# Optimization experiments

Hardware: AMD Instinct MI355X
Metric: run time of the kernel (lower is better)

The kernel has to match this reference:

```python
import jax, jax.numpy as jnp
import numpy as np

M_LOCAL = 100000
N_GLOBAL = 50000
C = 128
E = 1600000
EDGE_DIM = 16
BN_EPS = 1e-5


def setup_inputs() -> dict:
    key = jax.random.key(0)
    ks = jax.random.split(key, 12)
    s = 1.0 / np.sqrt(C)
    inp = {
        "h_local": jax.random.normal(ks[0], (M_LOCAL, C), jnp.float32),
        "h_global": jax.random.normal(ks[1], (N_GLOBAL, C), jnp.float32),
        "ea_flat": jax.random.normal(ks[2], (E, EDGE_DIM), jnp.float32),
        # GIN MLP: Linear(C,C) -> ReLU -> Linear(C,C)
        "W1": jax.random.normal(ks[3], (C, C), jnp.float32) * s,
        "b1": jnp.zeros((C,), jnp.float32),
        "W2": jax.random.normal(ks[4], (C, C), jnp.float32) * s,
        "b2": jnp.zeros((C,), jnp.float32),
        "eps": jnp.zeros((), jnp.float32),  # GIN train_eps, init 0
        "gamma_l": jnp.ones((C,), jnp.float32),
        "beta_l": jnp.zeros((C,), jnp.float32),
        "gamma_g": jnp.ones((C,), jnp.float32),
        "beta_g": jnp.zeros((C,), jnp.float32),
        "intra_ei": jax.random.randint(ks[5], (2, E), 0, M_LOCAL, jnp.int32),
        "node_ids": jax.random.randint(ks[6], (M_LOCAL,), 0, N_GLOBAL, jnp.int32),
        "valid": jnp.ones((M_LOCAL,), jnp.bool_),
        "N_total": N_GLOBAL,
    }
    return inp


def _batchnorm(x, gamma, beta):
    # training-mode BN: biased batch statistics over node dim
    mu = jnp.mean(x, axis=0)
    var = jnp.mean((x - mu) ** 2, axis=0)
    return (x - mu) * jax.lax.rsqrt(var + BN_EPS) * gamma + beta


def reference(h_local, h_global, ea_flat, W1, b1, W2, b2, eps,
              gamma_l, beta_l, gamma_g, beta_g,
              intra_ei, node_ids, valid, N_total):
    M = h_local.shape[0]
    valid_f = valid.astype(h_local.dtype)[:, None]
    clamped = jnp.maximum(node_ids, 0)

    # inject global context, zero padding
    h_in = (h_local + h_global[clamped]) * valid_f

    # GINConv: mlp((1+eps)*x + sum_{j->i} x_j)   (ea_flat unused for 'gin')
    src, dst = intra_ei[0], intra_ei[1]
    agg = jax.ops.segment_sum(h_in[src], dst, num_segments=M)
    pre = (1.0 + eps) * h_in + agg
    h_local_new = jnp.maximum(pre @ W1 + b1, 0.0) @ W2 + b2
    h_local_new = h_local_new * valid_f

    # cross-subgraph consensus: scatter mean into global nodes
    h_sum = jax.ops.segment_sum(h_local_new, clamped, num_segments=N_total)
    v_cnt = jax.ops.segment_sum(valid_f[:, 0], clamped, num_segments=N_total)
    h_global_new = h_sum / jnp.maximum(v_cnt, 1.0)[:, None]

    # local track: BN + residual (Identity since in==out) + mask (dropout p=0)
    h_local_new = _batchnorm(h_local_new, gamma_l, beta_l) + h_local
    h_local_new = h_local_new * valid_f

    # global track: BN + residual
    h_global_new = _batchnorm(h_global_new, gamma_g, beta_g) + h_global

    return (h_local_new, h_global_new)
```

## Files before the change

### kernel.cpp

```cpp
#include <hip/hip_runtime.h>

#define CDIM 128
#define NBE 3125
#define NBN 391
#define SMAXE 1024
#define SMAXN 512
#define CHUNK 16384
#define H1LD 136

typedef __bf16 bf16x8 __attribute__((ext_vector_type(8)));
typedef __bf16 bf16x4 __attribute__((ext_vector_type(4)));
typedef float f32x4 __attribute__((ext_vector_type(4)));

__global__ __launch_bounds__(256) void k_init(
    const float* __restrict__ hl, const float* __restrict__ hg,
    const int* __restrict__ nid, __bf16* __restrict__ h_in,
    const float* __restrict__ W1, const float* __restrict__ W2,
    __bf16* __restrict__ Wt1, __bf16* __restrict__ Wt2, int M, int gInit)
{
    int bid = blockIdx.x;
    if (bid >= gInit) {
        int idx = (bid - gInit) * 256 + threadIdx.x;
        int k = idx >> 7, n = idx & 127;
        Wt1[n * CDIM + k] = (__bf16)W1[k * CDIM + n];
        Wt2[n * CDIM + k] = (__bf16)W2[k * CDIM + n];
        return;
    }
    int idx = bid * 256 + threadIdx.x;
    if (idx >= M * 16) return;
    int i = idx >> 4, q8 = idx & 15;
    int g = max(nid[i], 0);
    const float4* hl4 = reinterpret_cast<const float4*>(hl);
    const float4* hg4 = reinterpret_cast<const float4*>(hg);
    float4 a0 = hl4[i * 32 + q8 * 2], a1 = hl4[i * 32 + q8 * 2 + 1];
    float4 b0 = hg4[g * 32 + q8 * 2], b1 = hg4[g * 32 + q8 * 2 + 1];
    bf16x8 o;
    o[0] = (__bf16)(a0.x + b0.x); o[1] = (__bf16)(a0.y + b0.y);
    o[2] = (__bf16)(a0.z + b0.z); o[3] = (__bf16)(a0.w + b0.w);
    o[4] = (__bf16)(a1.x + b1.x); o[5] = (__bf16)(a1.y + b1.y);
    o[6] = (__bf16)(a1.z + b1.z); o[7] = (__bf16)(a1.w + b1.w);
    *reinterpret_cast<bf16x8*>(&h_in[(size_t)i * CDIM + q8 * 8]) = o;
}

__global__ __launch_bounds__(256) void k_count(
    const int* __restrict__ ei, const int* __restrict__ nid,
    int* __restrict__ bcnt, int E, int M)
{
    __shared__ int lh[4608];
    int t = threadIdx.x;
    for (int i = t; i < 4608; i += 256) lh[i] = 0;
    __syncthreads();
    int stride = gridDim.x * 256;
    for (int e = blockIdx.x * 256 + t; e < E; e += stride)
        atomicAdd(&lh[ei[E + e] >> 5], 1);
    for (int i = blockIdx.x * 256 + t; i < M; i += stride)
        atomicAdd(&lh[4096 + (max(nid[i], 0) >> 7)], 1);
    __syncthreads();
    for (int i = t; i < 4608; i += 256)
        if (lh[i]) atomicAdd(&bcnt[i], lh[i]);
}

__global__ __launch_bounds__(1024) void k_scan(
    const int* __restrict__ bcnt, int* __restrict__ bboff_e,
    int* __restrict__ bboff_n, int* __restrict__ bcur)
{
    __shared__ int sh[1024];
    int t = threadIdx.x;
    int v0 = bcnt[4 * t], v1 = bcnt[4 * t + 1], v2 = bcnt[4 * t + 2], v3 = bcnt[4 * t + 3];
    int s = v0 + v1 + v2 + v3;
    sh[t] = s;
    __syncthreads();
    for (int st = 1; st < 1024; st <<= 1) {
        int a = (t >= st) ? sh[t - st] : 0;
        __syncthreads();
        sh[t] += a;
        __syncthreads();
    }
    int acc = sh[t] - s;
    bboff_e[4 * t] = acc; bcur[4 * t] = acc; acc += v0;
    bboff_e[4 * t + 1] = acc; bcur[4 * t + 1] = acc; acc += v1;
    bboff_e[4 * t + 2] = acc; bcur[4 * t + 2] = acc; acc += v2;
    bboff_e[4 * t + 3] = acc; bcur[4 * t + 3] = acc; acc += v3;
    if (t == 1023) bboff_e[4096] = acc;
    __syncthreads();
    int v = (t < 512) ? bcnt[4096 + t] : 0;
    sh[t] = v;
    __syncthreads();
    for (int st = 1; st < 1024; st <<= 1) {
        int a = (t >= st) ? sh[t - st] : 0;
        __syncthreads();
        sh[t] += a;
        __syncthreads();
    }
    int ex = sh[t] - v;
    if (t < 512) { bboff_n[t] = ex; bcur[4096 + t] = ex; }
    if (t == 511) bboff_n[512] = ex + v;
}

__global__ __launch_bounds__(256) void k_bscatter(
    const int* __restrict__ ei, const int* __restrict__ nid,
    int* __restrict__ bcur, int* __restrict__ packed_e,
    int* __restrict__ packed_n, int E, int M)
{
    __shared__ int lh[4608];
    int t = threadIdx.x;
    int e0 = blockIdx.x * CHUNK;
    int n = min(CHUNK, E - e0);
    for (int i = t; i < 4608; i += 256) lh[i] = 0;
    __syncthreads();
    for (int j = t; j < n; j += 256)
        atomicAdd(&lh[ei[E + e0 + j] >> 5], 1);
    for (int i = blockIdx.x * 256 + t; i < M; i += gridDim.x * 256)
        atomicAdd(&lh[4096 + (max(nid[i], 0) >> 7)], 1);
    __syncthreads();
    for (int i = t; i < 4608; i += 256) {
        int c = lh[i];
        if (c) lh[i] = atomicAdd(&bcur[i], c);
    }
    __syncthreads();
    for (int j = t; j < n; j += 256) {
        int s = ei[e0 + j], d = ei[E + e0 + j];
        int pos = atomicAdd(&lh[d >> 5], 1);
        packed_e[pos] = s | ((d & 31) << 17);
    }
    for (int i = blockIdx.x * 256 + t; i < M; i += gridDim.x * 256) {
        int g = max(nid[i], 0);
        int pos = atomicAdd(&lh[4096 + (g >> 7)], 1);
        packed_n[pos] = i | ((g & 127) << 17);
    }
}

__global__ __launch_bounds__(256) void k_agg_fused(
    const __bf16* __restrict__ h_in, const int* __restrict__ packed,
    const int* __restrict__ bboff, const float* __restrict__ epsp,
    __bf16* __restrict__ pre, int M)
{
    __shared__ int lsrc[SMAXE];
    __shared__ int lcnt[32], lbase[32], lpos[32];
    int t = threadIdx.x;
    int b = blockIdx.x;
    int base = bboff[b];
    int n = min(bboff[b + 1] - base, SMAXE);
    if (t < 32) lcnt[t] = 0;
    __syncthreads();
    for (int j = t; j < n; j += 256)
        atomicAdd(&lcnt[packed[base + j] >> 17], 1);
    __syncthreads();
    if (t == 0) {
        int acc = 0;
        for (int i = 0; i < 32; ++i) { int c = lcnt[i]; lbase[i] = acc; lpos[i] = acc; acc += c; }
    }
    __syncthreads();
    for (int j = t; j < n; j += 256) {
        int p = packed[base + j];
        int r = atomicAdd(&lpos[p >> 17], 1);
        lsrc[r] = p & 0x1FFFF;
    }
    __syncthreads();

    float es = 1.0f + epsp[0];
    int slot = t >> 4, q = t & 15;
    int r0 = b * 32;
#pragma unroll
    for (int rr0 = 0; rr0 < 2; ++rr0) {
        int rr = slot + rr0 * 16;
        int row = r0 + rr;
        if (row >= M) break;
        bf16x8 a = *reinterpret_cast<const bf16x8*>(&h_in[(size_t)row * CDIM + q * 8]);
        float f[8];
#pragma unroll
        for (int k2 = 0; k2 < 8; ++k2) f[k2] = es * (float)a[k2];
        int sb = lbase[rr], cnt = lcnt[rr];
        int j = 0;
        for (; j + 1 < cnt; j += 2) {
            int s0 = lsrc[sb + j], s1 = lsrc[sb + j + 1];
            bf16x8 u0 = *reinterpret_cast<const bf16x8*>(&h_in[(size_t)s0 * CDIM + q * 8]);
            bf16x8 u1 = *reinterpret_cast<const bf16x8*>(&h_in[(size_t)s1 * CDIM + q * 8]);
#pragma unroll
            for (int k2 = 0; k2 < 8; ++k2) f[k2] += (float)u0[k2] + (float)u1[k2];
        }
        if (j < cnt) {
            int s0 = lsrc[sb + j];
            bf16x8 u0 = *reinterpret_cast<const bf16x8*>(&h_in[(size_t)s0 * CDIM + q * 8]);
#pragma unroll
            for (int k2 = 0; k2 < 8; ++k2) f[k2] += (float)u0[k2];
        }
        bf16x8 o;
#pragma unroll
        for (int k2 = 0; k2 < 8; ++k2) o[k2] = (__bf16)f[k2];
        *reinterpret_cast<bf16x8*>(&pre[(size_t)row * CDIM + q * 8]) = o;
    }
}

__global__ __launch_bounds__(256) void k_mlp(
    const __bf16* __restrict__ pre, const __bf16* __restrict__ Wt1,
    const __bf16* __restrict__ Wt2, const float* __restrict__ b1,
    const float* __restrict__ b2, __bf16* __restrict__ y,
    float* __restrict__ part, int M)
{
    __shared__ bf16x8 w_lds4[2048];
    __shared__ __bf16 h1t[64 * H1LD];
    __shared__ float pst[256];
    int t = threadIdx.x;
#pragma unroll
    for (int j = 0; j < 8; ++j) {
        int c = t + j * 256;
        int n = c >> 4, cr = c & 15, kc = cr >> 2, g = cr & 3;
        w_lds4[((n >> 4) * 4 + kc) * 64 + g * 16 + (n & 15)] =
            reinterpret_cast<const bf16x8*>(Wt1)[c];
    }
    if (t < 256) pst[t] = 0.f;
    __syncthreads();

    int wave = t >> 6, lane = t & 63;
    int r0 = blockIdx.x * 64 + wave * 16;
    int srcrow = min(r0 + (lane & 15), M - 1);
    int krow = (lane >> 4) * 8;
    int col = lane & 15;

    bf16x8 a[4];
#pragma unroll
    for (int kc = 0; kc < 4; ++kc)
        a[kc] = *reinterpret_cast<const bf16x8*>(
            &pre[(size_t)srcrow * CDIM + kc * 32 + krow]);

    f32x4 acc1[8] = {};
#pragma unroll
    for (int kc = 0; kc < 4; ++kc)
#pragma unroll
        for (int nt = 0; nt < 8; ++nt)
            acc1[nt] = __builtin_amdgcn_mfma_f32_16x16x32_bf16(
                a[kc], w_lds4[(nt * 4 + kc) * 64 + lane], acc1[nt], 0, 0, 0);

    int lrowb = wave * 16 + (lane >> 4) * 4;
#pragma unroll
    for (int nt = 0; nt < 8; ++nt) {
        float bv = b1[nt * 16 + col];
#pragma unroll
        for (int reg = 0; reg < 4; ++reg) {
            float v = fmaxf(acc1[nt][reg] + bv, 0.f);
            h1t[(lrowb + reg) * H1LD + nt * 16 + col] = (__bf16)v;
        }
    }
    __syncthreads();

#pragma unroll
    for (int j = 0; j < 8; ++j) {
        int c = t + j * 256;
        int n = c >> 4, cr = c & 15, kc = cr >> 2, g = cr & 3;
        w_lds4[((n >> 4) * 4 + kc) * 64 + g * 16 + (n & 15)] =
            reinterpret_cast<const bf16x8*>(Wt2)[c];
    }
    __syncthreads();

    int lrow = wave * 16 + (lane & 15);
    bf16x8 a2[4];
#pragma unroll
    for (int kc = 0; kc < 4; ++kc)
        a2[kc] = *reinterpret_cast<const bf16x8*>(&h1t[lrow * H1LD + kc * 32 + krow]);

    f32x4 acc2[8] = {};
#pragma unroll
    for (int kc = 0; kc < 4; ++kc)
#pragma unroll
        for (int nt = 0; nt < 8; ++nt)
            acc2[nt] = __builtin_amdgcn_mfma_f32_16x16x32_bf16(
                a2[kc], w_lds4[(nt * 4 + kc) * 64 + lane], acc2[nt], 0, 0, 0);

    int rowbase = r0 + (lane >> 4) * 4;
#pragma unroll
    for (int nt = 0; nt < 8; ++nt) {
        float bv = b2[nt * 16 + col];
        float s = 0.f, s2 = 0.f;
#pragma unroll
        for (int reg = 0; reg < 4; ++reg) {
            int row = rowbase + reg;
            float v = acc2[nt][reg] + bv;
            if (row < M) {
                y[(size_t)row * CDIM + nt * 16 + col] = (__bf16)v;
                s += v;
                s2 = fmaf(v, v, s2);
            }
        }
        s += __shfl_xor(s, 16); s += __shfl_xor(s, 32);
        s2 += __shfl_xor(s2, 16); s2 += __shfl_xor(s2, 32);
        if ((lane >> 4) == 0) {
            atomicAdd(&pst[nt * 16 + col], s);
            atomicAdd(&pst[128 + nt * 16 + col], s2);
        }
    }
    __syncthreads();
    if (t < 256) part[(size_t)blockIdx.x * 256 + t] = pst[t];
}

__global__ __launch_bounds__(256) void k_gmean(
    const __bf16* __restrict__ y, const int* __restrict__ packed,
    const int* __restrict__ bboff, float* __restrict__ out_g,
    float* __restrict__ part, int N)
{
    __shared__ int lrows[SMAXN];
    __shared__ int lcnt[32], lbase[32], lpos[32];
    __shared__ float pst[256];
    int t = threadIdx.x;
    int b = blockIdx.x >> 2;
    int quarter = blockIdx.x & 3;
    int base = bboff[b];
    int n = min(bboff[b + 1] - base, SMAXN);
    if (t < 32) lcnt[t] = 0;
    if (t < 256) pst[t] = 0.f;
    __syncthreads();
    for (int j = t; j < n; j += 256) {
        int ld = packed[base + j] >> 17;
        if ((ld >> 5) == quarter) atomicAdd(&lcnt[ld & 31], 1);
    }
    __syncthreads();
    if (t == 0) {
        int acc = 0;
        for (int i = 0; i < 32; ++i) { int c = lcnt[i]; lbase[i] = acc; lpos[i] = acc; acc += c; }
    }
    __syncthreads();
    for (int j = t; j < n; j += 256) {
        int p = packed[base + j];
        int ld = p >> 17;
        if ((ld >> 5) == quarter) {
            int r = atomicAdd(&lpos[ld & 31], 1);
            lrows[r] = p & 0x1FFFF;
        }
    }
    __syncthreads();

    int slot = t >> 4, q = t & 15;
    int g0 = b * 128 + quarter * 32;
    float csum[8] = {}, csq[8] = {};
#pragma unroll
    for (int rr0 = 0; rr0 < 2; ++rr0) {
        int rr = slot + rr0 * 16;
        int g = g0 + rr;
        if (g >= N) break;
        float f[8] = {};
        int sb = lbase[rr], cnt = lcnt[rr];
        for (int j = 0; j < cnt; ++j) {
            int r = lrows[sb + j];
            bf16x8 v = *reinterpret_cast<const bf16x8*>(&y[(size_t)r * CDIM + q * 8]);
#pragma unroll
            for (int k2 = 0; k2 < 8; ++k2) f[k2] += (float)v[k2];
        }
        float inv = 1.0f / fmaxf((float)cnt, 1.0f);
        float4 o0, o1;
        o0.x = f[0] * inv; o0.y = f[1] * inv; o0.z = f[2] * inv; o0.w = f[3] * inv;
        o1.x = f[4] * inv; o1.y = f[5] * inv; o1.z = f[6] * inv; o1.w = f[7] * inv;
        float* dst = out_g + (size_t)g * CDIM + q * 8;
        *reinterpret_cast<float4*>(dst) = o0;
        *reinterpret_cast<float4*>(dst + 4) = o1;
        float m[8] = {o0.x, o0.y, o0.z, o0.w, o1.x, o1.y, o1.z, o1.w};
#pragma unroll
        for (int k2 = 0; k2 < 8; ++k2) {
            csum[k2] += m[k2];
            csq[k2] = fmaf(m[k2], m[k2], csq[k2]);
        }
    }
#pragma unroll
    for (int k2 = 0; k2 < 8; ++k2) {
        atomicAdd(&pst[q * 8 + k2], csum[k2]);
        atomicAdd(&pst[128 + q * 8 + k2], csq[k2]);
    }
    __syncthreads();
    if (t < 256) part[(size_t)blockIdx.x * 256 + t] = pst[t];
}

__global__ __launch_bounds__(256) void k_reduce_scale(
    const float* __restrict__ part_l, int nl,
    const float* __restrict__ part_g, int ng,
    const float* __restrict__ gl, const float* __restrict__ bl,
    const float* __restrict__ gg, const float* __restrict__ bg,
    float* __restrict__ sc, int M, int N)
{
    int c = blockIdx.x;
    bool isL = c < 128;
    const float* part = isL ? part_l : part_g;
    int n = isL ? nl : ng;
    int col = isL ? c : c - 128;
    int t = threadIdx.x;
    float s1 = 0.f, s2 = 0.f;
    for (int i = t; i < n; i += 256) {
        const float* row = part + (size_t)i * 256;
        s1 += row[col];
        s2 += row[128 + col];
    }
    __shared__ float sh1[256], sh2[256];
    sh1[t] = s1; sh2[t] = s2;
    __syncthreads();
    for (int w = 128; w > 0; w >>= 1) {
        if (t < w) { sh1[t] += sh1[t + w]; sh2[t] += sh2[t + w]; }
        __syncthreads();
    }
    if (t == 0) {
        float cnt = isL ? (float)M : (float)N;
        float mu = sh1[0] / cnt;
        float var = sh2[0] / cnt - mu * mu;
        float gamma = isL ? gl[col] : gg[col];
        float beta  = isL ? bl[col] : bg[col];
        float sca = gamma * rsqrtf(var + 1e-5f);
        int off = isL ? 0 : 256;
        sc[off + col] = sca;
        sc[off + 128 + col] = beta - mu * sca;
    }
}

__global__ __launch_bounds__(256) void k_fin(
    const __bf16* __restrict__ y, const float* __restrict__ hl,
    float* __restrict__ out_l, float* __restrict__ out_g,
    const float* __restrict__ hg, const float* __restrict__ sc,
    int M, int N, int gFinL)
{
    int bid = blockIdx.x;
    if (bid < gFinL) {
        int idx = bid * 256 + threadIdx.x;
        if (idx >= M * 32) return;
        int q = idx & 31;
        float4 s4 = reinterpret_cast<const float4*>(sc)[q];
        float4 h4 = reinterpret_cast<const float4*>(sc + 128)[q];
        bf16x4 v = *reinterpret_cast<const bf16x4*>(&y[(size_t)idx * 4]);
        float4 r = reinterpret_cast<const float4*>(hl)[idx];
        reinterpret_cast<float4*>(out_l)[idx] = make_float4(
            fmaf((float)v[0], s4.x, h4.x) + r.x, fmaf((float)v[1], s4.y, h4.y) + r.y,
            fmaf((float)v[2], s4.z, h4.z) + r.z, fmaf((float)v[3], s4.w, h4.w) + r.w);
    } else {
        int idx = (bid - gFinL) * 256 + threadIdx.x;
        if (idx >= N * 32) return;
        int q = idx & 31;
        float4 s4 = reinterpret_cast<const float4*>(sc + 256)[q];
        float4 h4 = reinterpret_cast<const float4*>(sc + 384)[q];
        float4 v = reinterpret_cast<float4*>(out_g)[idx];
        float4 r = reinterpret_cast<const float4*>(hg)[idx];
        reinterpret_cast<float4*>(out_g)[idx] = make_float4(
            fmaf(v.x, s4.x, h4.x) + r.x, fmaf(v.y, s4.y, h4.y) + r.y,
            fmaf(v.z, s4.z, h4.z) + r.z, fmaf(v.w, s4.w, h4.w) + r.w);
    }
}

extern "C" void kernel_launch(void* const* d_in, const int* in_sizes, int n_in,
                              void* d_out, int out_size, void* d_ws, size_t ws_size,
                              hipStream_t stream)
{
    const float* h_local  = (const float*)d_in[0];
    const float* h_global = (const float*)d_in[1];
    const float* W1   = (const float*)d_in[3];
    const float* b1   = (const float*)d_in[4];
    const float* W2   = (const float*)d_in[5];
    const float* b2   = (const float*)d_in[6];
    const float* eps  = (const float*)d_in[7];
    const float* gl   = (const float*)d_in[8];
    const float* bl   = (const float*)d_in[9];
    const float* gg   = (const float*)d_in[10];
    const float* bg   = (const float*)d_in[11];
    const int*   ei   = (const int*)d_in[12];
    const int*   nid  = (const int*)d_in[13];

    const int M = in_sizes[13];
    const int N = in_sizes[1] / CDIM;
    const int E = in_sizes[12] / 2;
    const int gGemm = (M + 63) / 64;
    const int nGm   = NBN * 4;

    float* out_l = (float*)d_out;
    float* out_g = out_l + (size_t)M * CDIM;

    __bf16* pre = (__bf16*)d_out;

    char* odf = (char*)d_out + 26000000;
    int* packed_n = (int*)odf;
    int* bcnt     = packed_n + M;
    int* bboff_e  = bcnt + 4608;
    int* bboff_n  = bboff_e + 4097;
    int* bcur     = bboff_n + 513;
    float* part_l = (float*)((char*)d_out + 28000000);
    float* part_g = part_l + (size_t)gGemm * 256;

    int* packed_e = (int*)out_g;

    __bf16* h_in = (__bf16*)d_ws;
    __bf16* y    = (__bf16*)((char*)d_ws + 25600000);
    char*  wst   = (char*)d_ws + 51200000;
    __bf16* Wt1  = (__bf16*)wst;
    __bf16* Wt2  = Wt1 + CDIM * CDIM;
    float* sc    = (float*)(Wt2 + CDIM * CDIM);

    hipMemsetAsync(bcnt, 0, 4608 * sizeof(int), stream);

    int gInit = (M * 16 + 255) / 256;
    k_init<<<gInit + 64, 256, 0, stream>>>(h_local, h_global, nid, h_in,
                                           W1, W2, Wt1, Wt2, M, gInit);

    k_count<<<256, 256, 0, stream>>>(ei, nid, bcnt, E, M);
    k_scan<<<1, 1024, 0, stream>>>(bcnt, bboff_e, bboff_n, bcur);

    int gBS = (E + CHUNK - 1) / CHUNK;
    k_bscatter<<<gBS, 256, 0, stream>>>(ei, nid, bcur, packed_e, packed_n, E, M);

    k_agg_fused<<<NBE, 256, 0, stream>>>(h_in, packed_e, bboff_e, eps, pre, M);

    k_mlp<<<gGemm, 256, 0, stream>>>(pre, Wt1, Wt2, b1, b2, y, part_l, M);

    k_gmean<<<nGm, 256, 0, stream>>>(y, packed_n, bboff_n, out_g, part_g, N);

    k_reduce_scale<<<256, 256, 0, stream>>>(part_l, gGemm, part_g, nGm,
                                            gl, bl, gg, bg, sc, M, N);

    int gFinL = (M * 32 + 255) / 256;
    int gFinG = (N * 32 + 255) / 256;
    k_fin<<<gFinL + gFinG, 256, 0, stream>>>(y, h_local, out_l, out_g,
                                             h_global, sc, M, N, gFinL);
}
```

Before: 279.0 us.

## Replace count-scan bucketing with fixed-capacity bucket slots in a single scatter pass

Removes the separate histogram-count and prefix-scan kernels. Edges and node ids are now scattered straight into fixed-capacity bucket slots (1024 per destination bucket, 512 per global-node bucket), and the atomic cursors double as bucket counts for the aggregation and mean kernels. The scatter kernel also moves to 1024-thread blocks with half-size chunks. This saves two launches and a full extra pass over the edge destination indices. The cost is a sparser layout, and any bucket that exceeds its capacity silently drops entries, which the earlier code also clamped.

```diff
diff --git a/kernel.cpp b/kernel.cpp
--- a/kernel.cpp
+++ b/kernel.cpp
@@ -3,9 +3,9 @@
 #define CDIM 128
 #define NBE 3125
 #define NBN 391
-#define SMAXE 1024
-#define SMAXN 512
-#define CHUNK 16384
+#define CAPE 1024
+#define CAPN 512
+#define CHUNK 8192
 #define H1LD 136
 
 typedef __bf16 bf16x8 __attribute__((ext_vector_type(8)));
@@ -42,62 +42,7 @@
     *reinterpret_cast<bf16x8*>(&h_in[(size_t)i * CDIM + q8 * 8]) = o;
 }
 
-__global__ __launch_bounds__(256) void k_count(
-    const int* __restrict__ ei, const int* __restrict__ nid,
-    int* __restrict__ bcnt, int E, int M)
-{
-    __shared__ int lh[4608];
-    int t = threadIdx.x;
-    for (int i = t; i < 4608; i += 256) lh[i] = 0;
-    __syncthreads();
-    int stride = gridDim.x * 256;
-    for (int e = blockIdx.x * 256 + t; e < E; e += stride)
-        atomicAdd(&lh[ei[E + e] >> 5], 1);
-    for (int i = blockIdx.x * 256 + t; i < M; i += stride)
-        atomicAdd(&lh[4096 + (max(nid[i], 0) >> 7)], 1);
-    __syncthreads();
-    for (int i = t; i < 4608; i += 256)
-        if (lh[i]) atomicAdd(&bcnt[i], lh[i]);
-}
-
-__global__ __launch_bounds__(1024) void k_scan(
-    const int* __restrict__ bcnt, int* __restrict__ bboff_e,
-    int* __restrict__ bboff_n, int* __restrict__ bcur)
-{
-    __shared__ int sh[1024];
-    int t = threadIdx.x;
-    int v0 = bcnt[4 * t], v1 = bcnt[4 * t + 1], v2 = bcnt[4 * t + 2], v3 = bcnt[4 * t + 3];
-    int s = v0 + v1 + v2 + v3;
-    sh[t] = s;
-    __syncthreads();
-    for (int st = 1; st < 1024; st <<= 1) {
-        int a = (t >= st) ? sh[t - st] : 0;
-        __syncthreads();
-        sh[t] += a;
-        __syncthreads();
-    }
-    int acc = sh[t] - s;
-    bboff_e[4 * t] = acc; bcur[4 * t] = acc; acc += v0;
-    bboff_e[4 * t + 1] = acc; bcur[4 * t + 1] = acc; acc += v1;
-    bboff_e[4 * t + 2] = acc; bcur[4 * t + 2] = acc; acc += v2;
-    bboff_e[4 * t + 3] = acc; bcur[4 * t + 3] = acc; acc += v3;
-    if (t == 1023) bboff_e[4096] = acc;
-    __syncthreads();
-    int v = (t < 512) ? bcnt[4096 + t] : 0;
-    sh[t] = v;
-    __syncthreads();
-    for (int st = 1; st < 1024; st <<= 1) {
-        int a = (t >= st) ? sh[t - st] : 0;
-        __syncthreads();
-        sh[t] += a;
-        __syncthreads();
-    }
-    int ex = sh[t] - v;
-    if (t < 512) { bboff_n[t] = ex; bcur[4096 + t] = ex; }
-    if (t == 511) bboff_n[512] = ex + v;
-}
-
-__global__ __launch_bounds__(256) void k_bscatter(
+__global__ __launch_bounds__(1024) void k_bscatter(
     const int* __restrict__ ei, const int* __restrict__ nid,
     int* __restrict__ bcur, int* __restrict__ packed_e,
     int* __restrict__ packed_n, int E, int M)
@@ -106,41 +51,43 @@
     int t = threadIdx.x;
     int e0 = blockIdx.x * CHUNK;
     int n = min(CHUNK, E - e0);
-    for (int i = t; i < 4608; i += 256) lh[i] = 0;
-    __syncthreads();
-    for (int j = t; j < n; j += 256)
+    for (int i = t; i < 4608; i += 1024) lh[i] = 0;
+    __syncthreads();
+    for (int j = t; j < n; j += 1024)
         atomicAdd(&lh[ei[E + e0 + j] >> 5], 1);
-    for (int i = blockIdx.x * 256 + t; i < M; i += gridDim.x * 256)
+    for (int i = blockIdx.x * 1024 + t; i < M; i += gridDim.x * 1024)
         atomicAdd(&lh[4096 + (max(nid[i], 0) >> 7)], 1);
     __syncthreads();
-    for (int i = t; i < 4608; i += 256) {
+    for (int i = t; i < 4608; i += 1024) {
         int c = lh[i];
-        if (c) lh[i] = atomicAdd(&bcur[i], c);
-    }
-    __syncthreads();
-    for (int j = t; j < n; j += 256) {
+        lh[i] = c ? atomicAdd(&bcur[i], c) : 0;
+    }
+    __syncthreads();
+    for (int j = t; j < n; j += 1024) {
         int s = ei[e0 + j], d = ei[E + e0 + j];
-        int pos = atomicAdd(&lh[d >> 5], 1);
-        packed_e[pos] = s | ((d & 31) << 17);
-    }
-    for (int i = blockIdx.x * 256 + t; i < M; i += gridDim.x * 256) {
+        int b = d >> 5;
+        int off = atomicAdd(&lh[b], 1);
+        if (off < CAPE) packed_e[b * CAPE + off] = s | ((d & 31) << 17);
+    }
+    for (int i = blockIdx.x * 1024 + t; i < M; i += gridDim.x * 1024) {
         int g = max(nid[i], 0);
-        int pos = atomicAdd(&lh[4096 + (g >> 7)], 1);
-        packed_n[pos] = i | ((g & 127) << 17);
+        int b = g >> 7;
+        int off = atomicAdd(&lh[4096 + b], 1);
+        if (off < CAPN) packed_n[b * CAPN + off] = i | ((g & 127) << 17);
     }
 }
 
 __global__ __launch_bounds__(256) void k_agg_fused(
     const __bf16* __restrict__ h_in, const int* __restrict__ packed,
-    const int* __restrict__ bboff, const float* __restrict__ epsp,
+    const int* __restrict__ bcur, const float* __restrict__ epsp,
     __bf16* __restrict__ pre, int M)
 {
-    __shared__ int lsrc[SMAXE];
+    __shared__ int lsrc[CAPE];
     __shared__ int lcnt[32], lbase[32], lpos[32];
     int t = threadIdx.x;
     int b = blockIdx.x;
-    int base = bboff[b];
-    int n = min(bboff[b + 1] - base, SMAXE);
+    int base = b * CAPE;
+    int n = min(bcur[b], CAPE);
     if (t < 32) lcnt[t] = 0;
     __syncthreads();
     for (int j = t; j < n; j += 256)
@@ -295,17 +242,17 @@
 
 __global__ __launch_bounds__(256) void k_gmean(
     const __bf16* __restrict__ y, const int* __restrict__ packed,
-    const int* __restrict__ bboff, float* __restrict__ out_g,
+    const int* __restrict__ bcur, float* __restrict__ out_g,
     float* __restrict__ part, int N)
 {
-    __shared__ int lrows[SMAXN];
+    __shared__ int lrows[CAPN];
     __shared__ int lcnt[32], lbase[32], lpos[32];
     __shared__ float pst[256];
     int t = threadIdx.x;
     int b = blockIdx.x >> 2;
     int quarter = blockIdx.x & 3;
-    int base = bboff[b];
-    int n = min(bboff[b + 1] - base, SMAXN);
+    int base = b * CAPN;
+    int n = min(bcur[4096 + b], CAPN);
     if (t < 32) lcnt[t] = 0;
     if (t < 256) pst[t] = 0.f;
     __syncthreads();
@@ -468,14 +415,9 @@
 
     __bf16* pre = (__bf16*)d_out;
 
-    char* odf = (char*)d_out + 26000000;
-    int* packed_n = (int*)odf;
-    int* bcnt     = packed_n + M;
-    int* bboff_e  = bcnt + 4608;
-    int* bboff_n  = bboff_e + 4097;
-    int* bcur     = bboff_n + 513;
-    float* part_l = (float*)((char*)d_out + 28000000);
-    float* part_g = part_l + (size_t)gGemm * 256;
+    int*   packed_n = (int*)((char*)d_out + 26000000);
+    float* part_l   = (float*)((char*)d_out + 28000000);
+    float* part_g   = part_l + (size_t)gGemm * 256;
 
     int* packed_e = (int*)out_g;
 
@@ -485,24 +427,22 @@
     __bf16* Wt1  = (__bf16*)wst;
     __bf16* Wt2  = Wt1 + CDIM * CDIM;
     float* sc    = (float*)(Wt2 + CDIM * CDIM);
-
-    hipMemsetAsync(bcnt, 0, 4608 * sizeof(int), stream);
+    int*   bcur  = (int*)(sc + 512);
+
+    hipMemsetAsync(bcur, 0, 4608 * sizeof(int), stream);
 
     int gInit = (M * 16 + 255) / 256;
     k_init<<<gInit + 64, 256, 0, stream>>>(h_local, h_global, nid, h_in,
                                            W1, W2, Wt1, Wt2, M, gInit);
 
-    k_count<<<256, 256, 0, stream>>>(ei, nid, bcnt, E, M);
-    k_scan<<<1, 1024, 0, stream>>>(bcnt, bboff_e, bboff_n, bcur);
-
     int gBS = (E + CHUNK - 1) / CHUNK;
-    k_bscatter<<<gBS, 256, 0, stream>>>(ei, nid, bcur, packed_e, packed_n, E, M);
-
-    k_agg_fused<<<NBE, 256, 0, stream>>>(h_in, packed_e, bboff_e, eps, pre, M);
+    k_bscatter<<<gBS, 1024, 0, stream>>>(ei, nid, bcur, packed_e, packed_n, E, M);
+
+    k_agg_fused<<<NBE, 256, 0, stream>>>(h_in, packed_e, bcur, eps, pre, M);
 
     k_mlp<<<gGemm, 256, 0, stream>>>(pre, Wt1, Wt2, b1, b2, y, part_l, M);
 
-    k_gmean<<<nGm, 256, 0, stream>>>(y, packed_n, bboff_n, out_g, part_g, N);
+    k_gmean<<<nGm, 256, 0, stream>>>(y, packed_n, bcur, out_g, part_g, N);
 
     k_reduce_scale<<<256, 256, 0, stream>>>(part_l, gGemm, part_g, nGm,
                                             gl, bl, gg, bg, sc, M, N);
```

After: 234.3 us. 16.0% less time.
